# Kernel tuning notes

Measured on AMD Instinct MI355X. Metric: run time of the kernel, lower is better.

The kernel has to match this reference:

```python
import jax, jax.numpy as jnp
import numpy as np

N = 50000          # num member nodes == num provider nodes
E = 800000         # provider->member bipartite edges (avg degree 16)
IN_M = 128; IN_P = 128; HID = 128; HEADS = 4; LAT = 64
NEG = 0.2          # leaky_relu negative slope (PyG GATConv default)


def gat_conv(x, src, dst, W, a_src, a_dst, b, heads, ch):
    """PyG-style GATConv (eval mode, concat heads). x:[N,F], src/dst:[Etot]."""
    n = x.shape[0]
    h = (x @ W).reshape(n, heads, ch)                       # [N,H,C]
    s = jnp.sum(h * a_src, axis=-1)                         # [N,H]
    d = jnp.sum(h * a_dst, axis=-1)                         # [N,H]
    e = jax.nn.leaky_relu(s[src] + d[dst], NEG)             # [Etot,H]
    # segment softmax over edges grouped by destination node
    m = jax.ops.segment_max(e, dst, num_segments=n)
    p = jnp.exp(e - m[dst])
    z = jax.ops.segment_sum(p, dst, num_segments=n)
    alpha = p / (z[dst] + 1e-16)                            # [Etot,H]
    out = jax.ops.segment_sum(h[src] * alpha[..., None], dst, num_segments=n)
    return out.reshape(n, heads * ch) + b


def setup_inputs() -> dict:
    key = jax.random.key(0)
    ks = jax.random.split(key, 24)
    gl = lambda k, shape, fan: (jax.random.normal(k, shape, jnp.float32) / np.sqrt(fan).astype(np.float32))
    return {
        "x_member": jax.random.normal(ks[0], (N, IN_M), jnp.float32),
        "x_provider": jax.random.normal(ks[1], (N, IN_P), jnp.float32),
        "edge_index": jax.random.randint(ks[2], (2, E), 0, N),
        "W1_m": gl(ks[3], (IN_M, HID), IN_M),
        "a_src1_m": gl(ks[4], (HEADS, HID // HEADS), HID // HEADS),
        "a_dst1_m": gl(ks[5], (HEADS, HID // HEADS), HID // HEADS),
        "b1_m": jnp.zeros((HID,), jnp.float32),
        "W2_m": gl(ks[6], (HID, LAT), HID),
        "a_src2_m": gl(ks[7], (1, LAT), LAT),
        "a_dst2_m": gl(ks[8], (1, LAT), LAT),
        "b2_m": jnp.zeros((LAT,), jnp.float32),
        "W1_p": gl(ks[9], (IN_P, HID), IN_P),
        "a_src1_p": gl(ks[10], (HEADS, HID // HEADS), HID // HEADS),
        "a_dst1_p": gl(ks[11], (HEADS, HID // HEADS), HID // HEADS),
        "b1_p": jnp.zeros((HID,), jnp.float32),
        "W2_p": gl(ks[12], (HID, LAT), HID),
        "a_src2_p": gl(ks[13], (1, LAT), LAT),
        "a_dst2_p": gl(ks[14], (1, LAT), LAT),
        "b2_p": jnp.zeros((LAT,), jnp.float32),
        "Wd_m": gl(ks[15], (LAT, IN_M), LAT),
        "bd_m": jnp.zeros((IN_M,), jnp.float32),
        "Wd_p": gl(ks[16], (LAT, IN_P), LAT),
        "bd_p": jnp.zeros((IN_P,), jnp.float32),
    }


def reference(x_member, x_provider, edge_index,
              W1_m, a_src1_m, a_dst1_m, b1_m, W2_m, a_src2_m, a_dst2_m, b2_m,
              W1_p, a_src1_p, a_dst1_p, b1_p, W2_p, a_src2_p, a_dst2_p, b2_p,
              Wd_m, bd_m, Wd_p, bd_p):
    prov, memb = edge_index[0], edge_index[1]
    loop = jnp.arange(N)
    # member graph: self loops + (provider -> member); provider graph: reverse
    m_src = jnp.concatenate([loop, prov]); m_dst = jnp.concatenate([loop, memb])
    p_src = jnp.concatenate([loop, memb]); p_dst = jnp.concatenate([loop, prov])

    xm = jax.nn.elu(gat_conv(x_member, m_src, m_dst, W1_m, a_src1_m, a_dst1_m, b1_m, HEADS, HID // HEADS))
    z_m = gat_conv(xm, m_src, m_dst, W2_m, a_src2_m, a_dst2_m, b2_m, 1, LAT)

    xp = jax.nn.elu(gat_conv(x_provider, p_src, p_dst, W1_p, a_src1_p, a_dst1_p, b1_p, HEADS, HID // HEADS))
    z_p = gat_conv(xp, p_src, p_dst, W2_p, a_src2_p, a_dst2_p, b2_p, 1, LAT)

    x_hat_member = z_m @ Wd_m + bd_m
    x_hat_provider = z_p @ Wd_p + bd_p
    edge_logits = jnp.sum(z_p[prov] * z_m[memb], axis=1)
    return (x_hat_member, x_hat_provider, edge_logits)
```

## Files before the change

### kernel.cpp

```cpp
#include <hip/hip_runtime.h>
#include <hip/hip_fp16.h>
#include <stdint.h>

typedef _Float16 f16_t;
typedef _Float16 f16x8 __attribute__((ext_vector_type(8)));
typedef float f32x4 __attribute__((ext_vector_type(4)));

__device__ __forceinline__ unsigned int pack_h2(float a, float b) {
    return (unsigned int)__half_as_ushort(__float2half(a)) |
           ((unsigned int)__half_as_ushort(__float2half(b)) << 16);
}
__device__ __forceinline__ float4 cvt_h4(uint2 r) {
    __half2 h0 = *reinterpret_cast<__half2*>(&r.x);
    __half2 h1 = *reinterpret_cast<__half2*>(&r.y);
    float2 f0 = __half22float2(h0), f1 = __half22float2(h1);
    return make_float4(f0.x, f0.y, f1.x, f1.y);
}

__global__ __launch_bounds__(256) void prep_kernel(
    const float* __restrict__ W1m, const float* __restrict__ as1m, const float* __restrict__ ad1m,
    const float* __restrict__ W1p, const float* __restrict__ as1p, const float* __restrict__ ad1p,
    const float* __restrict__ W2m, const float* __restrict__ as2m, const float* __restrict__ ad2m,
    const float* __restrict__ W2p, const float* __restrict__ as2p, const float* __restrict__ ad2p,
    const float* __restrict__ Wdm, const float* __restrict__ Wdp,
    f16_t* __restrict__ B1m, f16_t* __restrict__ B1p,
    f16_t* __restrict__ B2m, f16_t* __restrict__ B2p,
    f16_t* __restrict__ Bdm, f16_t* __restrict__ Bdp)
{
    const float *W = nullptr, *as = nullptr, *ad = nullptr;
    f16_t* B = nullptr; int K = 0, COUT = 0, H = 0;
    switch (blockIdx.x) {
        case 0: W = W1m; as = as1m; ad = ad1m; B = B1m; K = 128; COUT = 128; H = 4; break;
        case 1: W = W1p; as = as1p; ad = ad1p; B = B1p; K = 128; COUT = 128; H = 4; break;
        case 2: W = W2m; as = as2m; ad = ad2m; B = B2m; K = 128; COUT = 64;  H = 1; break;
        case 3: W = W2p; as = as2p; ad = ad2p; B = B2p; K = 128; COUT = 64;  H = 1; break;
        case 4: W = Wdm; B = Bdm; K = 64; COUT = 128; H = 0; break;
        case 5: W = Wdp; B = Bdp; K = 64; COUT = 128; H = 0; break;
    }
    const int total = (COUT + 16) * K;
    for (int idx = threadIdx.x; idx < total; idx += 256) {
        int c = idx / K, k = idx - c * K;
        float v = 0.f;
        if (c < COUT) {
            v = W[(size_t)k * COUT + c];
        } else {
            int e = c - COUT;
            if (H > 0 && e < 2 * H) {
                int h = (e < H) ? e : e - H;
                const float* av = (e < H) ? as : ad;
                int CH = COUT / H;
                for (int cc = 0; cc < CH; ++cc)
                    v += W[(size_t)k * COUT + h * CH + cc] * av[h * CH + cc];
            }
        }
        B[idx] = (f16_t)v;
    }
}

template<int K, int COUT, bool IN_HALF, bool OUT_HALF, int SDH, bool ADD_BIAS>
__global__ __launch_bounds__(256) void mfma_gemm(const void* __restrict__ X0,
                                                 const void* __restrict__ X1,
                                                 const f16_t* __restrict__ B0,
                                                 const f16_t* __restrict__ B1,
                                                 const float* __restrict__ b0,
                                                 const float* __restrict__ b1,
                                                 float* __restrict__ s_out,
                                                 float* __restrict__ d_out,
                                                 void* __restrict__ out0,
                                                 void* __restrict__ out1, int n)
{
    constexpr int NT = COUT / 16;
    constexpr int TT = NT + ((SDH > 0) ? 1 : 0);

    const int side = blockIdx.y;
    const void*  Xv = side ? X1 : X0;
    const f16_t* B  = side ? B1 : B0;
    const float* bias = side ? b1 : b0;
    void* outp = side ? out1 : out0;

    const int wid  = threadIdx.x >> 6;
    const int lane = threadIdx.x & 63;
    const int r0 = blockIdx.x * 64 + wid * 16;
    if (r0 >= n) return;
    const int col = lane & 15;
    const int kg  = lane >> 4;
    const int arow = min(r0 + col, n - 1);

    f32x4 acc[TT];
    #pragma unroll
    for (int t = 0; t < TT; ++t) acc[t] = (f32x4)0.f;

    #pragma unroll
    for (int kb = 0; kb < K; kb += 32) {
        f16x8 a;
        if constexpr (IN_HALF) {
            a = *reinterpret_cast<const f16x8*>((const f16_t*)Xv + (size_t)arow * K + kb + kg * 8);
        } else {
            const float* xp = (const float*)Xv + (size_t)arow * K + kb + kg * 8;
            float4 u = *reinterpret_cast<const float4*>(xp);
            float4 w = *reinterpret_cast<const float4*>(xp + 4);
            a[0] = (f16_t)u.x; a[1] = (f16_t)u.y; a[2] = (f16_t)u.z; a[3] = (f16_t)u.w;
            a[4] = (f16_t)w.x; a[5] = (f16_t)w.y; a[6] = (f16_t)w.z; a[7] = (f16_t)w.w;
        }
        #pragma unroll
        for (int t = 0; t < TT; ++t) {
            f16x8 bf = *reinterpret_cast<const f16x8*>(B + (size_t)(t * 16 + col) * K + kb + kg * 8);
            acc[t] = __builtin_amdgcn_mfma_f32_16x16x32_f16(a, bf, acc[t], 0, 0, 0);
        }
    }

    const int rb = r0 + 4 * (lane >> 4);
    #pragma unroll
    for (int t = 0; t < NT; ++t) {
        float bv = 0.f;
        if constexpr (ADD_BIAS) bv = bias[t * 16 + col];
        #pragma unroll
        for (int j = 0; j < 4; ++j) {
            int row = rb + j;
            if (row < n) {
                float v = acc[t][j] + bv;
                if constexpr (OUT_HALF)
                    ((__half*)outp)[(size_t)row * COUT + t * 16 + col] = __float2half(v);
                else
                    ((float*)outp)[(size_t)row * COUT + t * 16 + col] = v;
            }
        }
    }
    if constexpr (SDH > 0) {
        #pragma unroll
        for (int j = 0; j < 4; ++j) {
            int row = rb + j;
            if (row < n) {
                float v = acc[NT][j];
                size_t gi = (size_t)(side ? n + row : row) * SDH;
                if (col < SDH) s_out[gi + col] = v;
                else if (col < 2 * SDH) d_out[gi + (col - SDH)] = v;
            }
        }
    }
}

#define BSH 7
#define BCAP 2560
#define CHUNK_E 4096

__global__ __launch_bounds__(256) void bucket_scatter_kernel(const int* __restrict__ prov,
                                                             const int* __restrict__ memb,
                                                             int* __restrict__ bcnt,
                                                             int2* __restrict__ bstore,
                                                             int e, int n, int nbuck)
{
    __shared__ int hist[1024];
    __shared__ int lbase[1024];
    const int tid = threadIdx.x;
    const int e0 = blockIdx.x * CHUNK_E;
    const int e1 = min(e, e0 + CHUNK_E);

    for (int i = tid; i < nbuck; i += 256) hist[i] = 0;
    __syncthreads();
    for (int t = e0 + tid; t < e1; t += 256) {
        int m = memb[t], p = prov[t];
        atomicAdd(&hist[m >> BSH], 1);
        atomicAdd(&hist[(n + p) >> BSH], 1);
    }
    __syncthreads();
    for (int i = tid; i < nbuck; i += 256) {
        int h = hist[i];
        lbase[i] = (h > 0) ? atomicAdd(&bcnt[i], h) : 0;
        hist[i] = 0;
    }
    __syncthreads();
    for (int t = e0 + tid; t < e1; t += 256) {
        int m = memb[t], p = prov[t];
        int b1 = m >> BSH;
        int pos1 = lbase[b1] + atomicAdd(&hist[b1], 1);
        if (pos1 < BCAP) bstore[(size_t)b1 * BCAP + pos1] = make_int2(m, p);
        int d2 = n + p;
        int b2 = d2 >> BSH;
        int pos2 = lbase[b2] + atomicAdd(&hist[b2], 1);
        if (pos2 < BCAP) bstore[(size_t)b2 * BCAP + pos2] = make_int2(d2, m);
    }
}

__global__ __launch_bounds__(1024) void bucket_scan_kernel(const int* __restrict__ bcnt,
                                                           int* __restrict__ bbase,
                                                           int* __restrict__ roff,
                                                           int nb, int n2)
{
    __shared__ int tmp[1024];
    int tid = threadIdx.x;
    int v = (tid < nb) ? min(bcnt[tid], BCAP) : 0;
    tmp[tid] = v; __syncthreads();
    for (int o = 1; o < 1024; o <<= 1) {
        int x = (tid >= o) ? tmp[tid - o] : 0;
        __syncthreads();
        tmp[tid] += x;
        __syncthreads();
    }
    bbase[tid] = tmp[tid] - v;
    if (tid == 0) roff[n2] = tmp[1023];
}

__global__ __launch_bounds__(256) void bucket_build_kernel(const int* __restrict__ bcnt,
                                                           const int* __restrict__ bbase,
                                                           const int2* __restrict__ bstore,
                                                           int* __restrict__ roff,
                                                           int* __restrict__ colA,
                                                           int n2)
{
    __shared__ int2 ent[BCAP];
    __shared__ int  colL[BCAP];
    __shared__ int  cnts[128], pref[128], curs[128];

    const int b = blockIdx.x, tid = threadIdx.x;
    const int node0 = b << BSH;
    const int cnt  = min(bcnt[b], BCAP);
    const int base = bbase[b];

    if (tid < 128) cnts[tid] = 0;
    __syncthreads();
    for (int i = tid; i < cnt; i += 256) {
        int2 v = bstore[(size_t)b * BCAP + i];
        ent[i] = v;
        atomicAdd(&cnts[v.x - node0], 1);
    }
    __syncthreads();
    if (tid < 128) pref[tid] = cnts[tid];
    __syncthreads();
    #pragma unroll
    for (int o = 1; o < 128; o <<= 1) {
        int x = 0;
        if (tid < 128 && tid >= o) x = pref[tid - o];
        __syncthreads();
        if (tid < 128) pref[tid] += x;
        __syncthreads();
    }
    if (tid < 128) {
        int node = node0 + tid;
        if (node < n2) roff[node] = base + pref[tid] - cnts[tid];
        curs[tid] = 0;
    }
    __syncthreads();
    for (int i = tid; i < cnt; i += 256) {
        int2 v = ent[i];
        int loc = v.x - node0;
        int slot = (pref[loc] - cnts[loc]) + atomicAdd(&curs[loc], 1);
        colL[slot] = v.y;
    }
    __syncthreads();
    for (int i = tid; i < cnt; i += 256) colA[base + i] = colL[i];
}

template<int H>
__device__ __forceinline__ void store_alpha(__half* __restrict__ A, size_t e, const float* a) {
    if constexpr (H == 4) {
        uint2 w; w.x = pack_h2(a[0], a[1]); w.y = pack_h2(a[2], a[3]);
        *reinterpret_cast<uint2*>(A + e * 4) = w;
    } else {
        A[e] = __float2half(a[0]);
    }
}

template<int H>
__device__ __forceinline__ void alpha_one_fullwave(int iG, int lane,
                                                   const float* __restrict__ sarr,
                                                   const float* __restrict__ sb,
                                                   const float* __restrict__ darr,
                                                   const int* __restrict__ roff,
                                                   const int* __restrict__ col,
                                                   __half* __restrict__ A,
                                                   __half* __restrict__ aselfA)
{
    const int start = roff[iG], end = roff[iG + 1];
    const int deg = end - start;

    float dh[H], es[H];
    #pragma unroll
    for (int hh = 0; hh < H; ++hh) {
        dh[hh] = darr[(size_t)iG * H + hh];
        float e = sarr[(size_t)iG * H + hh] + dh[hh];
        es[hh] = fmaxf(e, 0.2f * e);
    }

    if (deg <= 64) {
        int srcL = (lane < deg) ? col[start + lane] : 0;
        float pl[H];
        if (lane < deg) {
            #pragma unroll
            for (int hh = 0; hh < H; ++hh) {
                float e = sb[(size_t)srcL * H + hh] + dh[hh];
                pl[hh] = __expf(fmaxf(e, 0.2f * e));
            }
        } else {
            #pragma unroll
            for (int hh = 0; hh < H; ++hh) pl[hh] = 0.f;
        }
        float zh[H];
        #pragma unroll
        for (int hh = 0; hh < H; ++hh) zh[hh] = pl[hh];
        #pragma unroll
        for (int hh = 0; hh < H; ++hh)
            for (int o = 32; o >= 1; o >>= 1)
                zh[hh] += __shfl_xor(zh[hh], o, 64);
        float av[H], sf[H];
        #pragma unroll
        for (int hh = 0; hh < H; ++hh) {
            float se = __expf(es[hh]);
            float invz = 1.f / (zh[hh] + se + 1e-16f);
            sf[hh] = se * invz;
            av[hh] = pl[hh] * invz;
        }
        if (lane < deg) store_alpha<H>(A, (size_t)(start + lane), av);
        if (lane == 0) store_alpha<H>(aselfA, (size_t)iG, sf);
        return;
    }

    float zh[H];
    #pragma unroll
    for (int hh = 0; hh < H; ++hh) zh[hh] = 0.f;
    for (int base = start; base < end; base += 64) {
        int idx = base + lane;
        if (idx < end) {
            int src = col[idx];
            #pragma unroll
            for (int hh = 0; hh < H; ++hh) {
                float e = sb[(size_t)src * H + hh] + dh[hh];
                e = fmaxf(e, 0.2f * e);
                zh[hh] += __expf(e);
            }
        }
    }
    #pragma unroll
    for (int hh = 0; hh < H; ++hh)
        for (int o = 32; o >= 1; o >>= 1)
            zh[hh] += __shfl_xor(zh[hh], o, 64);
    float invz[H], sf[H];
    #pragma unroll
    for (int hh = 0; hh < H; ++hh) {
        float se = __expf(es[hh]);
        invz[hh] = 1.f / (zh[hh] + se + 1e-16f);
        sf[hh] = se * invz[hh];
    }
    if (lane == 0) store_alpha<H>(aselfA, (size_t)iG, sf);
    for (int base = start; base < end; base += 64) {
        int idx = base + lane;
        if (idx < end) {
            int src = col[idx];
            float av[H];
            #pragma unroll
            for (int hh = 0; hh < H; ++hh) {
                float e = sb[(size_t)src * H + hh] + dh[hh];
                e = fmaxf(e, 0.2f * e);
                av[hh] = __expf(e) * invz[hh];
            }
            store_alpha<H>(A, (size_t)idx, av);
        }
    }
}

template<int H>
__global__ __launch_bounds__(256) void alpha_kernel(const float* __restrict__ sarr,
                                                    const float* __restrict__ darr,
                                                    const int* __restrict__ roff,
                                                    const int* __restrict__ col,
                                                    __half* __restrict__ A,
                                                    __half* __restrict__ aselfA, int N)
{
    const int n2 = 2 * N;
    const int lane = threadIdx.x & 63;
    const int g = lane >> 5, l = lane & 31;
    const int nw  = (gridDim.x * 256) >> 6;
    const int wv0 = (blockIdx.x * 256 + threadIdx.x) >> 6;
    const int npair = (n2 + 1) >> 1;

    for (int pr = wv0; pr < npair; pr += nw) {
        const int i0 = pr * 2;
        const bool nval = (i0 + g) < n2;
        const int iN = nval ? (i0 + g) : (n2 - 1);
        const int start = roff[iN], end = roff[iN + 1];
        const int deg = nval ? (end - start) : 0;
        const int degO = __shfl_xor(deg, 32, 64);

        if (max(deg, degO) <= 32) {
            const int side = (iN >= N) ? 1 : 0;
            const float* sb = sarr + (size_t)side * N * H;
            float dh[H], es[H];
            if constexpr (H == 4) {
                float4 dv = *reinterpret_cast<const float4*>(darr + (size_t)iN * 4);
                float4 sv = *reinterpret_cast<const float4*>(sarr + (size_t)iN * 4);
                dh[0] = dv.x; dh[1] = dv.y; dh[2] = dv.z; dh[3] = dv.w;
                float ev[4] = {sv.x + dv.x, sv.y + dv.y, sv.z + dv.z, sv.w + dv.w};
                #pragma unroll
                for (int hh = 0; hh < 4; ++hh) es[hh] = fmaxf(ev[hh], 0.2f * ev[hh]);
            } else {
                #pragma unroll
                for (int hh = 0; hh < H; ++hh) {
                    dh[hh] = darr[(size_t)iN * H + hh];
                    float e = sarr[(size_t)iN * H + hh] + dh[hh];
                    es[hh] = fmaxf(e, 0.2f * e);
                }
            }
            int srcL = (l < deg) ? col[start + l] : 0;
            float pl[H];
            if (l < deg) {
                if constexpr (H == 4) {
                    float4 sv = *reinterpret_cast<const float4*>(sb + (size_t)srcL * 4);
                    float ee[4] = {sv.x + dh[0], sv.y + dh[1], sv.z + dh[2], sv.w + dh[3]};
                    #pragma unroll
                    for (int hh = 0; hh < 4; ++hh) pl[hh] = __expf(fmaxf(ee[hh], 0.2f * ee[hh]));
                } else {
                    #pragma unroll
                    for (int hh = 0; hh < H; ++hh) {
                        float e = sb[(size_t)srcL * H + hh] + dh[hh];
                        pl[hh] = __expf(fmaxf(e, 0.2f * e));
                    }
                }
            } else {
                #pragma unroll
                for (int hh = 0; hh < H; ++hh) pl[hh] = 0.f;
            }
            float zh[H];
            #pragma unroll
            for (int hh = 0; hh < H; ++hh) zh[hh] = pl[hh];
            #pragma unroll
            for (int hh = 0; hh < H; ++hh)
                #pragma unroll
                for (int o = 16; o >= 1; o >>= 1)
                    zh[hh] += __shfl_xor(zh[hh], o, 64);
            float av[H], sf[H];
            #pragma unroll
            for (int hh = 0; hh < H; ++hh) {
                float se = __expf(es[hh]);
                float invz = 1.f / (zh[hh] + se + 1e-16f);
                sf[hh] = se * invz;
                av[hh] = pl[hh] * invz;
            }
            if (l < deg) store_alpha<H>(A, (size_t)(start + l), av);
            if (l == 0 && nval) store_alpha<H>(aselfA, (size_t)iN, sf);
        } else {
            for (int nd = 0; nd < 2; ++nd) {
                int i = i0 + nd;
                if (i >= n2) break;
                int sd2 = (i >= N) ? 1 : 0;
                alpha_one_fullwave<H>(i, lane, sarr, sarr + (size_t)sd2 * N * H, darr,
                                      roff, col, A, aselfA);
            }
        }
    }
}

template<int C, int H, bool ELU, bool OUTH>
__global__ __launch_bounds__(256) void gather_kernel(const __half* __restrict__ hm,
                                                     const __half* __restrict__ hp,
                                                     const __half* __restrict__ A,
                                                     const __half* __restrict__ aselfA,
                                                     const int* __restrict__ roff,
                                                     const int* __restrict__ col,
                                                     const float* __restrict__ bias_m,
                                                     const float* __restrict__ bias_p,
                                                     void* __restrict__ out_m,
                                                     void* __restrict__ out_p, int N)
{
    constexpr int CH  = C / H;
    constexpr int LRd = C / 8;
    constexpr int EPd = 32 / LRd;
    const int n2 = 2 * N;
    const int lane = threadIdx.x & 63;
    const int g = lane >> 5, l = lane & 31;
    const int sub = l / LRd, q = l % LRd;
    const int c0 = q * 8;
    const int hd = c0 / CH;
    const int nw  = (gridDim.x * 256) >> 6;
    const int wv0 = (blockIdx.x * 256 + threadIdx.x) >> 6;
    const int npair = (n2 + 1) >> 1;

    for (int pr = wv0; pr < npair; pr += nw) {
        const int i0 = pr * 2;
        const bool nval = (i0 + g) < n2;
        const int iN = nval ? (i0 + g) : (n2 - 1);
        const int side = (iN >= N) ? 1 : 0;
        const int lN = iN - side * N;
        const __half* hf = side ? hp : hm;
        const int start = roff[iN];
        const int deg = roff[iN + 1] - start;

        float acc[8];
        #pragma unroll
        for (int j = 0; j < 8; ++j) acc[j] = 0.f;
        if (sub == 0) {
            uint4 r = *reinterpret_cast<const uint4*>(hf + (size_t)lN * C + c0);
            float4 lo = cvt_h4(make_uint2(r.x, r.y));
            float4 hi = cvt_h4(make_uint2(r.z, r.w));
            float a = __half2float(aselfA[(size_t)iN * H + hd]);
            acc[0] = a * lo.x; acc[1] = a * lo.y; acc[2] = a * lo.z; acc[3] = a * lo.w;
            acc[4] = a * hi.x; acc[5] = a * hi.y; acc[6] = a * hi.z; acc[7] = a * hi.w;
        }
        int t = sub;
#define GSTEP(U)                                                                     \
        while (t + (U - 1) * EPd < deg) {                                            \
            int ss[U]; float aa[U]; uint4 rr[U];                                     \
            _Pragma("unroll")                                                        \
            for (int u = 0; u < U; ++u) {                                            \
                int e = start + t + u * EPd;                                         \
                ss[u] = col[e];                                                      \
                aa[u] = __half2float(A[(size_t)e * H + hd]);                         \
            }                                                                        \
            _Pragma("unroll")                                                        \
            for (int u = 0; u < U; ++u)                                              \
                rr[u] = *reinterpret_cast<const uint4*>(hf + (size_t)ss[u] * C + c0); \
            _Pragma("unroll")                                                        \
            for (int u = 0; u < U; ++u) {                                            \
                float4 lo = cvt_h4(make_uint2(rr[u].x, rr[u].y));                    \
                float4 hi = cvt_h4(make_uint2(rr[u].z, rr[u].w));                    \
                acc[0] = fmaf(aa[u], lo.x, acc[0]);                                  \
                acc[1] = fmaf(aa[u], lo.y, acc[1]);                                  \
                acc[2] = fmaf(aa[u], lo.z, acc[2]);                                  \
                acc[3] = fmaf(aa[u], lo.w, acc[3]);                                  \
                acc[4] = fmaf(aa[u], hi.x, acc[4]);                                  \
                acc[5] = fmaf(aa[u], hi.y, acc[5]);                                  \
                acc[6] = fmaf(aa[u], hi.z, acc[6]);                                  \
                acc[7] = fmaf(aa[u], hi.w, acc[7]);                                  \
            }                                                                        \
            t += U * EPd;                                                            \
        }
        GSTEP(4)
        GSTEP(2)
        GSTEP(1)
#undef GSTEP
        #pragma unroll
        for (int o = LRd; o < 32; o <<= 1) {
            #pragma unroll
            for (int j = 0; j < 8; ++j) acc[j] += __shfl_xor(acc[j], o, 64);
        }
        if (sub == 0 && nval) {
            const float* biasS = side ? bias_p : bias_m;
            float4 b0 = *reinterpret_cast<const float4*>(biasS + c0);
            float4 b1 = *reinterpret_cast<const float4*>(biasS + c0 + 4);
            float v[8] = {acc[0] + b0.x, acc[1] + b0.y, acc[2] + b0.z, acc[3] + b0.w,
                          acc[4] + b1.x, acc[5] + b1.y, acc[6] + b1.z, acc[7] + b1.w};
            if constexpr (ELU) {
                #pragma unroll
                for (int j = 0; j < 8; ++j) v[j] = (v[j] > 0.f) ? v[j] : (__expf(v[j]) - 1.f);
            }
            if constexpr (OUTH) {
                __half* outS = (__half*)(side ? out_p : out_m);
                uint4 w;
                w.x = pack_h2(v[0], v[1]); w.y = pack_h2(v[2], v[3]);
                w.z = pack_h2(v[4], v[5]); w.w = pack_h2(v[6], v[7]);
                *reinterpret_cast<uint4*>(outS + (size_t)lN * C + c0) = w;
            } else {
                float* outS = (float*)(side ? out_p : out_m);
                float* po = outS + (size_t)lN * C + c0;
                *reinterpret_cast<float4*>(po)     = make_float4(v[0], v[1], v[2], v[3]);
                *reinterpret_cast<float4*>(po + 4) = make_float4(v[4], v[5], v[6], v[7]);
            }
        }
    }
}

__global__ __launch_bounds__(256) void logits_kernel(const __half* __restrict__ zp,
                                                     const __half* __restrict__ zm,
                                                     const int* __restrict__ prov,
                                                     const int* __restrict__ memb,
                                                     float* __restrict__ outv, int e)
{
    const int nw   = (gridDim.x * 256) >> 6;
    const int wv   = (blockIdx.x * 256 + threadIdx.x) >> 6;
    const int lane = threadIdx.x & 63;
    const int g = lane >> 3, q = lane & 7;
    const int c0 = q * 8;
    for (int base = wv * 16; base < e; base += nw * 16) {
        int e1 = base + g, e2 = base + 8 + g;
        bool v1 = e1 < e, v2 = e2 < e;
        int i1 = v1 ? e1 : (e - 1), i2 = v2 ? e2 : (e - 1);
        int p1 = prov[i1], m1 = memb[i1];
        int p2 = prov[i2], m2 = memb[i2];
        uint4 a1 = *reinterpret_cast<const uint4*>(zp + (size_t)p1 * 64 + c0);
        uint4 b1 = *reinterpret_cast<const uint4*>(zm + (size_t)m1 * 64 + c0);
        uint4 a2 = *reinterpret_cast<const uint4*>(zp + (size_t)p2 * 64 + c0);
        uint4 b2 = *reinterpret_cast<const uint4*>(zm + (size_t)m2 * 64 + c0);
        float4 al1 = cvt_h4(make_uint2(a1.x, a1.y)), ah1 = cvt_h4(make_uint2(a1.z, a1.w));
        float4 bl1 = cvt_h4(make_uint2(b1.x, b1.y)), bh1 = cvt_h4(make_uint2(b1.z, b1.w));
        float4 al2 = cvt_h4(make_uint2(a2.x, a2.y)), ah2 = cvt_h4(make_uint2(a2.z, a2.w));
        float4 bl2 = cvt_h4(make_uint2(b2.x, b2.y)), bh2 = cvt_h4(make_uint2(b2.z, b2.w));
        float s1 = al1.x * bl1.x + al1.y * bl1.y + al1.z * bl1.z + al1.w * bl1.w
                 + ah1.x * bh1.x + ah1.y * bh1.y + ah1.z * bh1.z + ah1.w * bh1.w;
        float s2 = al2.x * bl2.x + al2.y * bl2.y + al2.z * bl2.z + al2.w * bl2.w
                 + ah2.x * bh2.x + ah2.y * bh2.y + ah2.z * bh2.z + ah2.w * bh2.w;
        #pragma unroll
        for (int o = 1; o < 8; o <<= 1) {
            s1 += __shfl_xor(s1, o, 64);
            s2 += __shfl_xor(s2, o, 64);
        }
        if (q == 0) {
            if (v1) outv[e1] = s1;
            if (v2) outv[e2] = s2;
        }
    }
}

extern "C" void kernel_launch(void* const* d_in, const int* in_sizes, int n_in,
                              void* d_out, int out_size, void* d_ws, size_t ws_size,
                              hipStream_t stream)
{
    const int N_ = in_sizes[0] / 128;
    const int E_ = in_sizes[2] / 2;

    const float* x_member   = (const float*)d_in[0];
    const float* x_provider = (const float*)d_in[1];
    const int*   prov = (const int*)d_in[2];
    const int*   memb = prov + E_;
    const float* W1_m = (const float*)d_in[3];
    const float* a_src1_m = (const float*)d_in[4];
    const float* a_dst1_m = (const float*)d_in[5];
    const float* b1_m = (const float*)d_in[6];
    const float* W2_m = (const float*)d_in[7];
    const float* a_src2_m = (const float*)d_in[8];
    const float* a_dst2_m = (const float*)d_in[9];
    const float* b2_m = (const float*)d_in[10];
    const float* W1_p = (const float*)d_in[11];
    const float* a_src1_p = (const float*)d_in[12];
    const float* a_dst1_p = (const float*)d_in[13];
    const float* b1_p = (const float*)d_in[14];
    const float* W2_p = (const float*)d_in[15];
    const float* a_src2_p = (const float*)d_in[16];
    const float* a_dst2_p = (const float*)d_in[17];
    const float* b2_p = (const float*)d_in[18];
    const float* Wd_m = (const float*)d_in[19];
    const float* bd_m = (const float*)d_in[20];
    const float* Wd_p = (const float*)d_in[21];
    const float* bd_p = (const float*)d_in[22];

    const int n2 = 2 * N_;
    const int NB = (n2 + 127) >> BSH;

    char* p = (char*)d_ws;
    auto alloc = [&](size_t bytes) { void* q = (void*)p; p += (bytes + 255) & ~(size_t)255; return q; };
    __half* h1m   = (__half*)alloc((size_t)N_ * 128 * 2);
    __half* h1p   = (__half*)alloc((size_t)N_ * 128 * 2);
    __half* xm16m = (__half*)alloc((size_t)N_ * 128 * 2);
    __half* xm16p = (__half*)alloc((size_t)N_ * 128 * 2);
    __half* zm16  = (__half*)alloc((size_t)N_ * 64 * 2);
    __half* zp16  = (__half*)alloc((size_t)N_ * 64 * 2);
    float* s1     = (float*)alloc((size_t)n2 * 4 * 4);
    float* d1     = (float*)alloc((size_t)n2 * 4 * 4);
    __half* alpha2= (__half*)alloc((size_t)2 * E_ * 2);
    __half* aselfH= (__half*)alloc((size_t)n2 * 4 * 2);
    int*   bcnt   = (int*)alloc((size_t)NB * 4);
    int*   bbase  = (int*)alloc(1024 * 4);
    int*   roff2  = (int*)alloc((size_t)(n2 + 1) * 4);
    int*   colA   = (int*)alloc((size_t)2 * E_ * 4);
    f16_t* B1m = (f16_t*)alloc((size_t)(128 + 16) * 128 * 2);
    f16_t* B1p = (f16_t*)alloc((size_t)(128 + 16) * 128 * 2);
    f16_t* B2m = (f16_t*)alloc((size_t)(64 + 16) * 128 * 2);
    f16_t* B2p = (f16_t*)alloc((size_t)(64 + 16) * 128 * 2);
    f16_t* Bdm = (f16_t*)alloc((size_t)(128 + 16) * 64 * 2);
    f16_t* Bdp = (f16_t*)alloc((size_t)(128 + 16) * 64 * 2);
    __half* h2m = h1m;
    __half* h2p = h1p;
    int2*  bstore = (int2*)h1m;
    __half* alpha1 = zm16;

    hipMemsetAsync(bcnt, 0, (size_t)NB * 4, stream);
    bucket_scatter_kernel<<<(E_ + CHUNK_E - 1) / CHUNK_E, 256, 0, stream>>>(prov, memb, bcnt, bstore, E_, N_, NB);
    bucket_scan_kernel<<<1, 1024, 0, stream>>>(bcnt, bbase, roff2, NB, n2);
    bucket_build_kernel<<<NB, 256, 0, stream>>>(bcnt, bbase, bstore, roff2, colA, n2);

    prep_kernel<<<6, 256, 0, stream>>>(
        W1_m, a_src1_m, a_dst1_m, W1_p, a_src1_p, a_dst1_p,
        W2_m, a_src2_m, a_dst2_m, W2_p, a_src2_p, a_dst2_p,
        Wd_m, Wd_p, B1m, B1p, B2m, B2p, Bdm, Bdp);

    const dim3 gg((N_ + 63) / 64, 2);
    float* out = (float*)d_out;

    mfma_gemm<128, 128, false, true, 4, false><<<gg, 256, 0, stream>>>(
        x_member, x_provider, B1m, B1p, nullptr, nullptr, s1, d1, h1m, h1p, N_);
    alpha_kernel<4><<<2048, 256, 0, stream>>>(s1, d1, roff2, colA, alpha1, aselfH, N_);
    gather_kernel<128, 4, true, true><<<2048, 256, 0, stream>>>(
        h1m, h1p, alpha1, aselfH, roff2, colA, b1_m, b1_p, xm16m, xm16p, N_);

    mfma_gemm<128, 64, true, true, 1, false><<<gg, 256, 0, stream>>>(
        xm16m, xm16p, B2m, B2p, nullptr, nullptr, s1, d1, h2m, h2p, N_);
    alpha_kernel<1><<<2048, 256, 0, stream>>>(s1, d1, roff2, colA, alpha2, aselfH, N_);
    gather_kernel<64, 1, false, true><<<2048, 256, 0, stream>>>(
        h2m, h2p, alpha2, aselfH, roff2, colA, b2_m, b2_p, zm16, zp16, N_);

    mfma_gemm<64, 128, true, false, 0, true><<<gg, 256, 0, stream>>>(
        zm16, zp16, Bdm, Bdp, bd_m, bd_p, nullptr, nullptr,
        out, out + (size_t)N_ * 128, N_);
    logits_kernel<<<2048, 256, 0, stream>>>(zp16, zm16, prov, memb, out + (size_t)N_ * 128 * 2, E_);
}
```

Measured before the change: 455.9 us.

## Process two row tiles per wave and pre-swizzle weights into MFMA fragment layout

Each wave now computes 32 rows (two 16-row MFMA tiles) and reuses each loaded B fragment for both, halving weight-fragment loads per output row. The prep kernel writes weights in a lane-ordered fragment layout so each lane's B load is a single contiguous 16-byte read, fully coalesced across the wave. The grid is halved to match. Register use for accumulators doubles, and fewer blocks may reduce latency hiding.

```diff
diff --git a/kernel.cpp b/kernel.cpp
--- a/kernel.cpp
+++ b/kernel.cpp
@@ -37,17 +37,26 @@
         case 4: W = Wdm; B = Bdm; K = 64; COUT = 128; H = 0; break;
         case 5: W = Wdp; B = Bdp; K = 64; COUT = 128; H = 0; break;
     }
-    const int total = (COUT + 16) * K;
+    const int KB = K / 32;
+    const int TT = (COUT + 16) / 16;
+    const int total = TT * KB * 512;
     for (int idx = threadIdx.x; idx < total; idx += 256) {
-        int c = idx / K, k = idx - c * K;
+        int t    = idx / (KB * 512);
+        int r    = idx - t * (KB * 512);
+        int kb   = r >> 9;
+        int r2   = r & 511;
+        int lane = r2 >> 3, e = r2 & 7;
+        int col  = lane & 15, kg = lane >> 4;
+        int k    = kb * 32 + kg * 8 + e;
+        int c    = t * 16 + col;
         float v = 0.f;
         if (c < COUT) {
             v = W[(size_t)k * COUT + c];
         } else {
-            int e = c - COUT;
-            if (H > 0 && e < 2 * H) {
-                int h = (e < H) ? e : e - H;
-                const float* av = (e < H) ? as : ad;
+            int ee = c - COUT;
+            if (H > 0 && ee < 2 * H) {
+                int h = (ee < H) ? ee : ee - H;
+                const float* av = (ee < H) ? as : ad;
                 int CH = COUT / H;
                 for (int cc = 0; cc < CH; ++cc)
                     v += W[(size_t)k * COUT + h * CH + cc] * av[h * CH + cc];
@@ -71,6 +80,7 @@
 {
     constexpr int NT = COUT / 16;
     constexpr int TT = NT + ((SDH > 0) ? 1 : 0);
+    constexpr int KB = K / 32;
 
     const int side = blockIdx.y;
     const void*  Xv = side ? X1 : X0;
@@ -80,61 +90,74 @@
 
     const int wid  = threadIdx.x >> 6;
     const int lane = threadIdx.x & 63;
-    const int r0 = blockIdx.x * 64 + wid * 16;
+    const int r0 = blockIdx.x * 128 + wid * 32;
     if (r0 >= n) return;
     const int col = lane & 15;
     const int kg  = lane >> 4;
-    const int arow = min(r0 + col, n - 1);
-
-    f32x4 acc[TT];
+    const int ar0 = min(r0 + col, n - 1);
+    const int ar1 = min(r0 + 16 + col, n - 1);
+
+    f32x4 acc[2][TT];
     #pragma unroll
-    for (int t = 0; t < TT; ++t) acc[t] = (f32x4)0.f;
+    for (int h = 0; h < 2; ++h)
+        #pragma unroll
+        for (int t = 0; t < TT; ++t) acc[h][t] = (f32x4)0.f;
 
     #pragma unroll
-    for (int kb = 0; kb < K; kb += 32) {
-        f16x8 a;
+    for (int kb = 0; kb < KB; ++kb) {
+        f16x8 a0, a1;
         if constexpr (IN_HALF) {
-            a = *reinterpret_cast<const f16x8*>((const f16_t*)Xv + (size_t)arow * K + kb + kg * 8);
+            a0 = *reinterpret_cast<const f16x8*>((const f16_t*)Xv + (size_t)ar0 * K + kb * 32 + kg * 8);
+            a1 = *reinterpret_cast<const f16x8*>((const f16_t*)Xv + (size_t)ar1 * K + kb * 32 + kg * 8);
         } else {
-            const float* xp = (const float*)Xv + (size_t)arow * K + kb + kg * 8;
-            float4 u = *reinterpret_cast<const float4*>(xp);
-            float4 w = *reinterpret_cast<const float4*>(xp + 4);
-            a[0] = (f16_t)u.x; a[1] = (f16_t)u.y; a[2] = (f16_t)u.z; a[3] = (f16_t)u.w;
-            a[4] = (f16_t)w.x; a[5] = (f16_t)w.y; a[6] = (f16_t)w.z; a[7] = (f16_t)w.w;
+            const float* x0 = (const float*)Xv + (size_t)ar0 * K + kb * 32 + kg * 8;
+            const float* x1 = (const float*)Xv + (size_t)ar1 * K + kb * 32 + kg * 8;
+            float4 u0 = *reinterpret_cast<const float4*>(x0);
+            float4 w0 = *reinterpret_cast<const float4*>(x0 + 4);
+            float4 u1 = *reinterpret_cast<const float4*>(x1);
+            float4 w1 = *reinterpret_cast<const float4*>(x1 + 4);
+            a0[0] = (f16_t)u0.x; a0[1] = (f16_t)u0.y; a0[2] = (f16_t)u0.z; a0[3] = (f16_t)u0.w;
+            a0[4] = (f16_t)w0.x; a0[5] = (f16_t)w0.y; a0[6] = (f16_t)w0.z; a0[7] = (f16_t)w0.w;
+            a1[0] = (f16_t)u1.x; a1[1] = (f16_t)u1.y; a1[2] = (f16_t)u1.z; a1[3] = (f16_t)u1.w;
+            a1[4] = (f16_t)w1.x; a1[5] = (f16_t)w1.y; a1[6] = (f16_t)w1.z; a1[7] = (f16_t)w1.w;
         }
         #pragma unroll
         for (int t = 0; t < TT; ++t) {
-            f16x8 bf = *reinterpret_cast<const f16x8*>(B + (size_t)(t * 16 + col) * K + kb + kg * 8);
-            acc[t] = __builtin_amdgcn_mfma_f32_16x16x32_f16(a, bf, acc[t], 0, 0, 0);
-        }
-    }
-
-    const int rb = r0 + 4 * (lane >> 4);
+            f16x8 bf = *reinterpret_cast<const f16x8*>(B + ((size_t)(t * KB + kb) * 64 + lane) * 8);
+            acc[0][t] = __builtin_amdgcn_mfma_f32_16x16x32_f16(a0, bf, acc[0][t], 0, 0, 0);
+            acc[1][t] = __builtin_amdgcn_mfma_f32_16x16x32_f16(a1, bf, acc[1][t], 0, 0, 0);
+        }
+    }
+
     #pragma unroll
-    for (int t = 0; t < NT; ++t) {
-        float bv = 0.f;
-        if constexpr (ADD_BIAS) bv = bias[t * 16 + col];
-        #pragma unroll
-        for (int j = 0; j < 4; ++j) {
-            int row = rb + j;
-            if (row < n) {
-                float v = acc[t][j] + bv;
-                if constexpr (OUT_HALF)
-                    ((__half*)outp)[(size_t)row * COUT + t * 16 + col] = __float2half(v);
-                else
-                    ((float*)outp)[(size_t)row * COUT + t * 16 + col] = v;
-            }
-        }
-    }
-    if constexpr (SDH > 0) {
-        #pragma unroll
-        for (int j = 0; j < 4; ++j) {
-            int row = rb + j;
-            if (row < n) {
-                float v = acc[NT][j];
-                size_t gi = (size_t)(side ? n + row : row) * SDH;
-                if (col < SDH) s_out[gi + col] = v;
-                else if (col < 2 * SDH) d_out[gi + (col - SDH)] = v;
+    for (int h = 0; h < 2; ++h) {
+        const int rb = r0 + h * 16 + 4 * kg;
+        #pragma unroll
+        for (int t = 0; t < NT; ++t) {
+            float bv = 0.f;
+            if constexpr (ADD_BIAS) bv = bias[t * 16 + col];
+            #pragma unroll
+            for (int j = 0; j < 4; ++j) {
+                int row = rb + j;
+                if (row < n) {
+                    float v = acc[h][t][j] + bv;
+                    if constexpr (OUT_HALF)
+                        ((__half*)outp)[(size_t)row * COUT + t * 16 + col] = __float2half(v);
+                    else
+                        ((float*)outp)[(size_t)row * COUT + t * 16 + col] = v;
+                }
+            }
+        }
+        if constexpr (SDH > 0) {
+            #pragma unroll
+            for (int j = 0; j < 4; ++j) {
+                int row = rb + j;
+                if (row < n) {
+                    float v = acc[h][NT][j];
+                    size_t gi = (size_t)(side ? n + row : row) * SDH;
+                    if (col < SDH) s_out[gi + col] = v;
+                    else if (col < 2 * SDH) d_out[gi + (col - SDH)] = v;
+                }
             }
         }
     }
@@ -671,7 +694,7 @@
         W2_m, a_src2_m, a_dst2_m, W2_p, a_src2_p, a_dst2_p,
         Wd_m, Wd_p, B1m, B1p, B2m, B2p, Bdm, Bdp);
 
-    const dim3 gg((N_ + 63) / 64, 2);
+    const dim3 gg((N_ + 127) / 128, 2);
     float* out = (float*)d_out;
 
     mfma_gemm<128, 128, false, true, 4, false><<<gg, 256, 0, stream>>>(
```

Measured after the change: 445.4 us. 1.02x faster.
